# Performance work log

Measured on AMD Instinct MI355X. Metric: run time of the kernel, lower is better.

Reference implementation:

```python
import jax, jax.numpy as jnp
import numpy as np
import math

N, CIN, COUT, H, W, K = 8, 192, 192, 64, 64, 1024


def setup_inputs() -> dict:
    key = jax.random.key(0)
    k1, k2, k3, k4, k5 = jax.random.split(key, 5)
    latent = jax.random.normal(k1, (N, CIN, H, W), dtype=jnp.float32)
    # kaiming-uniform-like codebook init
    bound = math.sqrt(6.0 / COUT)
    codebook = jax.random.uniform(k2, (K, COUT), dtype=jnp.float32, minval=-bound, maxval=bound)
    # nn.Linear weights: [out_features, in_features]
    wq = jax.random.normal(k3, (COUT, CIN), dtype=jnp.float32) / math.sqrt(CIN)
    wk = jax.random.normal(k4, (COUT, COUT), dtype=jnp.float32) / math.sqrt(COUT)
    wv = jax.random.normal(k5, (COUT, COUT), dtype=jnp.float32) / math.sqrt(COUT)
    temperature1 = jnp.ones((), dtype=jnp.float32)
    return {"latent": latent, "codebook": codebook, "wq": wq, "wk": wk, "wv": wv,
            "temperature1": temperature1, "temperature": 1}


def reference(latent, codebook, wq, wk, wv, temperature1, temperature):
    # latent: [n, cin, h, w] -> q: [n, h, w, cout]
    q = jnp.einsum('nchw,oc->nhwo', latent, wq)
    k = codebook @ wk.T          # [K, cout]
    v = codebook @ wv.T          # [K, cout]
    scale = math.sqrt(CIN)
    # logit: [n, h, w, K]
    logit = jnp.einsum('nhwd,kd->nhwk', q, k) / scale * temperature1
    trueCode = jnp.argmax(logit, axis=-1)  # [n, h, w]
    # gumbel-softmax, hard=True (straight-through)
    gumbel = jax.random.gumbel(jax.random.key(42), logit.shape, dtype=logit.dtype)
    y_soft = jax.nn.softmax((logit + gumbel) / temperature, axis=-1)
    idx = jnp.argmax(y_soft, axis=-1)
    y_hard = jax.nn.one_hot(idx, K, dtype=logit.dtype)
    sample = y_hard + y_soft - jax.lax.stop_gradient(y_soft)
    # quantized: [n, h, w, cout] -> [n, cout, h, w]
    quantized = jnp.einsum('nhwk,kd->nhwd', sample, v).transpose(0, 3, 1, 2)
    return quantized, trueCode, logit
```

## Files before the change

kernel.cpp:

```cpp
#include <hip/hip_runtime.h>
#include <cstdint>
#include <cstddef>

#define CIN   192
#define COUT  192
#define KCB   1024
#define HWSZ  4096
#define NPIX  32768
#define LOGIT_SCALE_F 13.856406460551018f

#define QCOL0 832

__device__ __forceinline__ void threefry_0_42(uint32_t x0, uint32_t x1,
                                              uint32_t& o0, uint32_t& o1) {
  const uint32_t ks0 = 0u;
  const uint32_t ks1 = 42u;
  const uint32_t ks2 = 0x1BD11BDAu ^ 0u ^ 42u;
  x0 += ks0; x1 += ks1;
#define TFR(r) { x0 += x1; x1 = (x1 << (r)) | (x1 >> (32 - (r))); x1 ^= x0; }
  TFR(13) TFR(15) TFR(26) TFR(6)
  x0 += ks1; x1 += ks2 + 1u;
  TFR(17) TFR(29) TFR(16) TFR(24)
  x0 += ks2; x1 += ks0 + 2u;
  TFR(13) TFR(15) TFR(26) TFR(6)
  x0 += ks0; x1 += ks1 + 3u;
  TFR(17) TFR(29) TFR(16) TFR(24)
  x0 += ks1; x1 += ks2 + 4u;
  TFR(13) TFR(15) TFR(26) TFR(6)
  x0 += ks2; x1 += ks0 + 5u;
#undef TFR
  o0 = x0; o1 = x1;
}

__device__ __forceinline__ float gumbel_from_bits(uint32_t b) {
  float u = __uint_as_float((b >> 9) | 0x3F800000u) - 1.0f;
  u = fmaxf(u, 1.17549435e-38f);
  return -logf(-logf(u));
}

__global__ __launch_bounds__(192) void kv_kernel(
    const float* __restrict__ cb, const float* __restrict__ wk,
    const float* __restrict__ wv, float* __restrict__ km, float* __restrict__ vm) {
  __shared__ float4 row[48];
  const int j = blockIdx.x;
  const int o = threadIdx.x;
  if (o < 48) row[o] = reinterpret_cast<const float4*>(cb + (size_t)j * CIN)[o];
  __syncthreads();
  const float4* wkr = reinterpret_cast<const float4*>(wk + (size_t)o * CIN);
  const float4* wvr = reinterpret_cast<const float4*>(wv + (size_t)o * CIN);
  float sk = 0.f, sv = 0.f;
#pragma unroll 8
  for (int c = 0; c < 48; ++c) {
    float4 a = row[c];
    float4 b = wkr[c];
    float4 w = wvr[c];
    sk = fmaf(a.x, b.x, sk); sk = fmaf(a.y, b.y, sk);
    sk = fmaf(a.z, b.z, sk); sk = fmaf(a.w, b.w, sk);
    sv = fmaf(a.x, w.x, sv); sv = fmaf(a.y, w.y, sv);
    sv = fmaf(a.z, w.z, sv); sv = fmaf(a.w, w.w, sv);
  }
  km[(size_t)j * COUT + o] = sk;
  vm[(size_t)j * COUT + o] = sv;
}

__global__ __launch_bounds__(256) void q_kernel(
    const float* __restrict__ latent, const float* __restrict__ wq,
    float* __restrict__ logitq) {
  __shared__ float aT[16][68];
  __shared__ float bT[16][68];
  const int tid = threadIdx.x;
  const int p0 = blockIdx.x * 64;
  const int o0 = blockIdx.y * 64;
  const int n = p0 >> 12, hw0 = p0 & 4095;
  const float* lat = latent + (size_t)n * (CIN * HWSZ);
  const int tp = tid & 15, to = tid >> 4;
  float acc[4][4] = {};

  for (int c0 = 0; c0 < CIN; c0 += 16) {
    __syncthreads();
    {
      int px = tid & 63, cr = tid >> 6;
#pragma unroll
      for (int i = 0; i < 4; ++i) {
        int c = cr + i * 4;
        aT[c][px] = lat[(size_t)(c0 + c) * HWSZ + hw0 + px];
      }
      int tx = tid & 15, ty = tid >> 4;
#pragma unroll
      for (int i = 0; i < 4; ++i) {
        int o = ty * 4 + i;
        bT[tx][o] = wq[(size_t)(o0 + o) * CIN + c0 + tx];
      }
    }
    __syncthreads();
#pragma unroll
    for (int c = 0; c < 16; ++c) {
      float4 av = *reinterpret_cast<const float4*>(&aT[c][4 * tp]);
      float4 bv = *reinterpret_cast<const float4*>(&bT[c][4 * to]);
      acc[0][0] = fmaf(av.x, bv.x, acc[0][0]); acc[0][1] = fmaf(av.x, bv.y, acc[0][1]);
      acc[0][2] = fmaf(av.x, bv.z, acc[0][2]); acc[0][3] = fmaf(av.x, bv.w, acc[0][3]);
      acc[1][0] = fmaf(av.y, bv.x, acc[1][0]); acc[1][1] = fmaf(av.y, bv.y, acc[1][1]);
      acc[1][2] = fmaf(av.y, bv.z, acc[1][2]); acc[1][3] = fmaf(av.y, bv.w, acc[1][3]);
      acc[2][0] = fmaf(av.z, bv.x, acc[2][0]); acc[2][1] = fmaf(av.z, bv.y, acc[2][1]);
      acc[2][2] = fmaf(av.z, bv.z, acc[2][2]); acc[2][3] = fmaf(av.z, bv.w, acc[2][3]);
      acc[3][0] = fmaf(av.w, bv.x, acc[3][0]); acc[3][1] = fmaf(av.w, bv.y, acc[3][1]);
      acc[3][2] = fmaf(av.w, bv.z, acc[3][2]); acc[3][3] = fmaf(av.w, bv.w, acc[3][3]);
    }
  }
#pragma unroll
  for (int ii = 0; ii < 4; ++ii) {
    float4 w;
    w.x = acc[ii][0]; w.y = acc[ii][1]; w.z = acc[ii][2]; w.w = acc[ii][3];
    *reinterpret_cast<float4*>(logitq + (size_t)(p0 + 4 * tp + ii) * KCB + QCOL0 + o0 + 4 * to) = w;
  }
}

__global__ __launch_bounds__(256) void logit_kernel(
    const float* __restrict__ km, const float* __restrict__ vm,
    const float* __restrict__ t1p, float* __restrict__ logit_out,
    float* __restrict__ code_out, float* __restrict__ quant_out) {
  __shared__ float aT[CIN][68];
  __shared__ float bT[32][68];
  __shared__ float wLv[64][4];
  __shared__ int   wLi[64][4];
  __shared__ float wSv[64][4];
  __shared__ int   wSi[64][4];
  __shared__ int   sIdx[64];

  const int tid = threadIdx.x;
  const int p0 = blockIdx.x * 64;
  const float t1 = t1p[0];

  for (int i = 0; i < 12; ++i) {
    int flat = tid + i * 256;
    int r = flat / 48, c4 = flat % 48;
    float4 v = reinterpret_cast<const float4*>(
        logit_out + (size_t)(p0 + r) * KCB + QCOL0)[c4];
    aT[c4 * 4 + 0][r] = v.x;
    aT[c4 * 4 + 1][r] = v.y;
    aT[c4 * 4 + 2][r] = v.z;
    aT[c4 * 4 + 3][r] = v.w;
  }

  const int tp = tid & 15;
  const int to = tid >> 4;
  float Lv[4], Sv[4];
  int Li[4], Si[4];
#pragma unroll
  for (int ii = 0; ii < 4; ++ii) {
    Lv[ii] = -INFINITY; Sv[ii] = -INFINITY; Li[ii] = 0; Si[ii] = 0;
  }

  for (int jt = 0; jt < 16; ++jt) {
    float acc[4][4] = {};
    for (int c0 = 0; c0 < CIN; c0 += 32) {
      __syncthreads();
      {
        int c4 = tid & 7, jj = tid >> 3;
#pragma unroll
        for (int pass = 0; pass < 2; ++pass) {
          int jloc = jj + pass * 32;
          int jg = jt * 64 + jloc;
          float4 v = reinterpret_cast<const float4*>(km + (size_t)jg * CIN + c0)[c4];
          bT[c4 * 4 + 0][jloc] = v.x;
          bT[c4 * 4 + 1][jloc] = v.y;
          bT[c4 * 4 + 2][jloc] = v.z;
          bT[c4 * 4 + 3][jloc] = v.w;
        }
      }
      __syncthreads();
#pragma unroll
      for (int c = 0; c < 32; ++c) {
        float4 av = *reinterpret_cast<const float4*>(&aT[c0 + c][4 * tp]);
        float4 bv = *reinterpret_cast<const float4*>(&bT[c][4 * to]);
        acc[0][0] = fmaf(av.x, bv.x, acc[0][0]); acc[0][1] = fmaf(av.x, bv.y, acc[0][1]);
        acc[0][2] = fmaf(av.x, bv.z, acc[0][2]); acc[0][3] = fmaf(av.x, bv.w, acc[0][3]);
        acc[1][0] = fmaf(av.y, bv.x, acc[1][0]); acc[1][1] = fmaf(av.y, bv.y, acc[1][1]);
        acc[1][2] = fmaf(av.y, bv.z, acc[1][2]); acc[1][3] = fmaf(av.y, bv.w, acc[1][3]);
        acc[2][0] = fmaf(av.z, bv.x, acc[2][0]); acc[2][1] = fmaf(av.z, bv.y, acc[2][1]);
        acc[2][2] = fmaf(av.z, bv.z, acc[2][2]); acc[2][3] = fmaf(av.z, bv.w, acc[2][3]);
        acc[3][0] = fmaf(av.w, bv.x, acc[3][0]); acc[3][1] = fmaf(av.w, bv.y, acc[3][1]);
        acc[3][2] = fmaf(av.w, bv.z, acc[3][2]); acc[3][3] = fmaf(av.w, bv.w, acc[3][3]);
      }
    }
#pragma unroll
    for (int ii = 0; ii < 4; ++ii) {
      int p = p0 + 4 * tp + ii;
      int jb = jt * 64 + 4 * to;
      float4 lv;
      lv.x = acc[ii][0] / LOGIT_SCALE_F * t1;
      lv.y = acc[ii][1] / LOGIT_SCALE_F * t1;
      lv.z = acc[ii][2] / LOGIT_SCALE_F * t1;
      lv.w = acc[ii][3] / LOGIT_SCALE_F * t1;
      *reinterpret_cast<float4*>(logit_out + (size_t)p * KCB + jb) = lv;
      float vals[4] = {lv.x, lv.y, lv.z, lv.w};
#pragma unroll
      for (int jj = 0; jj < 4; ++jj) {
        int jgl = jb + jj;
        float val = vals[jj];
        if (val > Lv[ii]) { Lv[ii] = val; Li[ii] = jgl; }
        uint32_t b0, b1;
        threefry_0_42(0u, (uint32_t)p * (uint32_t)KCB + (uint32_t)jgl, b0, b1);
        float s = val + gumbel_from_bits(b0 ^ b1);
        if (s > Sv[ii]) { Sv[ii] = s; Si[ii] = jgl; }
      }
    }
  }

  {
    const int lane = tid & 63;
    const int wvid = tid >> 6;
#pragma unroll
    for (int ii = 0; ii < 4; ++ii) {
      float v = Lv[ii]; int idx = Li[ii];
      float s = Sv[ii]; int sidx = Si[ii];
#pragma unroll
      for (int m = 16; m <= 32; m <<= 1) {
        float v2 = __shfl_xor(v, m); int i2 = __shfl_xor(idx, m);
        if (v2 > v || (v2 == v && i2 < idx)) { v = v2; idx = i2; }
        float s2 = __shfl_xor(s, m); int j2 = __shfl_xor(sidx, m);
        if (s2 > s || (s2 == s && j2 < sidx)) { s = s2; sidx = j2; }
      }
      if (lane < 16) {
        int r = 4 * tp + ii;
        wLv[r][wvid] = v; wLi[r][wvid] = idx;
        wSv[r][wvid] = s; wSi[r][wvid] = sidx;
      }
    }
  }
  __syncthreads();
  if (tid < 64) {
    int r = tid;
    float bv = wLv[r][0]; int bi = wLi[r][0];
    float sv = wSv[r][0]; int si = wSi[r][0];
#pragma unroll
    for (int t = 1; t < 4; ++t) {
      float v1 = wLv[r][t]; int i1 = wLi[r][t];
      if (v1 > bv || (v1 == bv && i1 < bi)) { bv = v1; bi = i1; }
      float v2 = wSv[r][t]; int i2 = wSi[r][t];
      if (v2 > sv || (v2 == sv && i2 < si)) { sv = v2; si = i2; }
    }
    code_out[p0 + r] = (float)bi;
    sIdx[r] = si;
  }
  __syncthreads();

  {
    int l = tid & 63, dg = tid >> 6;
    int p = p0 + l;
    int n = p >> 12, hw = p & 4095;
    int jv = sIdx[l];
    const float* vrow = vm + (size_t)jv * COUT;
    float* qb = quant_out + (size_t)n * (COUT * HWSZ) + hw;
#pragma unroll
    for (int it = 0; it < 48; ++it) {
      int d = it * 4 + dg;
      qb[(size_t)d * HWSZ] = vrow[d];
    }
  }
}

extern "C" void kernel_launch(void* const* d_in, const int* in_sizes, int n_in,
                              void* d_out, int out_size, void* d_ws, size_t ws_size,
                              hipStream_t stream) {
  (void)in_sizes; (void)n_in; (void)out_size; (void)ws_size;
  const float* latent   = (const float*)d_in[0];
  const float* codebook = (const float*)d_in[1];
  const float* wq       = (const float*)d_in[2];
  const float* wk       = (const float*)d_in[3];
  const float* wv       = (const float*)d_in[4];
  const float* t1       = (const float*)d_in[5];

  float* ws = (float*)d_ws;
  float* km = ws;
  float* vm = ws + 196608;

  float* quant = (float*)d_out;
  float* code  = quant + 6291456;
  float* logit = code + 32768;

  kv_kernel<<<dim3(KCB), dim3(192), 0, stream>>>(codebook, wk, wv, km, vm);
  q_kernel<<<dim3(NPIX / 64, CIN / 64), dim3(256), 0, stream>>>(latent, wq, logit);
  logit_kernel<<<dim3(NPIX / 64), dim3(256), 0, stream>>>(km, vm, t1, logit, code, quant);
}
```

Baseline: 563.8 us.

## Fuse Q projection into logit kernel and double-buffer codebook key tiles

Computes the per-pixel Q projection directly into shared memory inside the logit kernel, removing the separate q_kernel and the scratch round-trip through the logit output buffer. It also double-buffers the key tile loads with register prefetch so global loads overlap the FMA loop, cutting one barrier per step, and adds a launch-bounds occupancy hint. In exchange each block recomputes Q for its 64 pixels, and the larger shared footprint plus prefetch registers may limit occupancy.

After: 872.3 us. 54.7% more time.

```diff
diff --git a/kernel.cpp b/kernel.cpp
--- a/kernel.cpp
+++ b/kernel.cpp
@@ -8,8 +8,6 @@
 #define HWSZ  4096
 #define NPIX  32768
 #define LOGIT_SCALE_F 13.856406460551018f
-
-#define QCOL0 832
 
 __device__ __forceinline__ void threefry_0_42(uint32_t x0, uint32_t x1,
                                               uint32_t& o0, uint32_t& o1) {
@@ -37,6 +35,17 @@
   u = fmaxf(u, 1.17549435e-38f);
   return -logf(-logf(u));
 }
+
+#define FMA16(acc, av, bv) do { \
+  acc[0][0]=fmaf(av.x,bv.x,acc[0][0]); acc[0][1]=fmaf(av.x,bv.y,acc[0][1]); \
+  acc[0][2]=fmaf(av.x,bv.z,acc[0][2]); acc[0][3]=fmaf(av.x,bv.w,acc[0][3]); \
+  acc[1][0]=fmaf(av.y,bv.x,acc[1][0]); acc[1][1]=fmaf(av.y,bv.y,acc[1][1]); \
+  acc[1][2]=fmaf(av.y,bv.z,acc[1][2]); acc[1][3]=fmaf(av.y,bv.w,acc[1][3]); \
+  acc[2][0]=fmaf(av.z,bv.x,acc[2][0]); acc[2][1]=fmaf(av.z,bv.y,acc[2][1]); \
+  acc[2][2]=fmaf(av.z,bv.z,acc[2][2]); acc[2][3]=fmaf(av.z,bv.w,acc[2][3]); \
+  acc[3][0]=fmaf(av.w,bv.x,acc[3][0]); acc[3][1]=fmaf(av.w,bv.y,acc[3][1]); \
+  acc[3][2]=fmaf(av.w,bv.z,acc[3][2]); acc[3][3]=fmaf(av.w,bv.w,acc[3][3]); \
+} while (0)
 
 __global__ __launch_bounds__(192) void kv_kernel(
     const float* __restrict__ cb, const float* __restrict__ wk,
@@ -63,64 +72,13 @@
   vm[(size_t)j * COUT + o] = sv;
 }
 
-__global__ __launch_bounds__(256) void q_kernel(
+__global__ __launch_bounds__(256, 2) void fused_kernel(
     const float* __restrict__ latent, const float* __restrict__ wq,
-    float* __restrict__ logitq) {
-  __shared__ float aT[16][68];
-  __shared__ float bT[16][68];
-  const int tid = threadIdx.x;
-  const int p0 = blockIdx.x * 64;
-  const int o0 = blockIdx.y * 64;
-  const int n = p0 >> 12, hw0 = p0 & 4095;
-  const float* lat = latent + (size_t)n * (CIN * HWSZ);
-  const int tp = tid & 15, to = tid >> 4;
-  float acc[4][4] = {};
-
-  for (int c0 = 0; c0 < CIN; c0 += 16) {
-    __syncthreads();
-    {
-      int px = tid & 63, cr = tid >> 6;
-#pragma unroll
-      for (int i = 0; i < 4; ++i) {
-        int c = cr + i * 4;
-        aT[c][px] = lat[(size_t)(c0 + c) * HWSZ + hw0 + px];
-      }
-      int tx = tid & 15, ty = tid >> 4;
-#pragma unroll
-      for (int i = 0; i < 4; ++i) {
-        int o = ty * 4 + i;
-        bT[tx][o] = wq[(size_t)(o0 + o) * CIN + c0 + tx];
-      }
-    }
-    __syncthreads();
-#pragma unroll
-    for (int c = 0; c < 16; ++c) {
-      float4 av = *reinterpret_cast<const float4*>(&aT[c][4 * tp]);
-      float4 bv = *reinterpret_cast<const float4*>(&bT[c][4 * to]);
-      acc[0][0] = fmaf(av.x, bv.x, acc[0][0]); acc[0][1] = fmaf(av.x, bv.y, acc[0][1]);
-      acc[0][2] = fmaf(av.x, bv.z, acc[0][2]); acc[0][3] = fmaf(av.x, bv.w, acc[0][3]);
-      acc[1][0] = fmaf(av.y, bv.x, acc[1][0]); acc[1][1] = fmaf(av.y, bv.y, acc[1][1]);
-      acc[1][2] = fmaf(av.y, bv.z, acc[1][2]); acc[1][3] = fmaf(av.y, bv.w, acc[1][3]);
-      acc[2][0] = fmaf(av.z, bv.x, acc[2][0]); acc[2][1] = fmaf(av.z, bv.y, acc[2][1]);
-      acc[2][2] = fmaf(av.z, bv.z, acc[2][2]); acc[2][3] = fmaf(av.z, bv.w, acc[2][3]);
-      acc[3][0] = fmaf(av.w, bv.x, acc[3][0]); acc[3][1] = fmaf(av.w, bv.y, acc[3][1]);
-      acc[3][2] = fmaf(av.w, bv.z, acc[3][2]); acc[3][3] = fmaf(av.w, bv.w, acc[3][3]);
-    }
-  }
-#pragma unroll
-  for (int ii = 0; ii < 4; ++ii) {
-    float4 w;
-    w.x = acc[ii][0]; w.y = acc[ii][1]; w.z = acc[ii][2]; w.w = acc[ii][3];
-    *reinterpret_cast<float4*>(logitq + (size_t)(p0 + 4 * tp + ii) * KCB + QCOL0 + o0 + 4 * to) = w;
-  }
-}
-
-__global__ __launch_bounds__(256) void logit_kernel(
     const float* __restrict__ km, const float* __restrict__ vm,
     const float* __restrict__ t1p, float* __restrict__ logit_out,
     float* __restrict__ code_out, float* __restrict__ quant_out) {
   __shared__ float aT[CIN][68];
-  __shared__ float bT[32][68];
+  __shared__ float bT[2][32][68];
   __shared__ float wLv[64][4];
   __shared__ int   wLi[64][4];
   __shared__ float wSv[64][4];
@@ -129,21 +87,49 @@
 
   const int tid = threadIdx.x;
   const int p0 = blockIdx.x * 64;
+  const int n = p0 >> 12, hw0 = p0 & 4095;
   const float t1 = t1p[0];
-
-  for (int i = 0; i < 12; ++i) {
-    int flat = tid + i * 256;
-    int r = flat / 48, c4 = flat % 48;
-    float4 v = reinterpret_cast<const float4*>(
-        logit_out + (size_t)(p0 + r) * KCB + QCOL0)[c4];
-    aT[c4 * 4 + 0][r] = v.x;
-    aT[c4 * 4 + 1][r] = v.y;
-    aT[c4 * 4 + 2][r] = v.z;
-    aT[c4 * 4 + 3][r] = v.w;
-  }
-
   const int tp = tid & 15;
   const int to = tid >> 4;
+
+  {
+    const float4* lat4 =
+        reinterpret_cast<const float4*>(latent + (size_t)n * (CIN * HWSZ));
+    const float4* wq4 = reinterpret_cast<const float4*>(wq);
+    const int hw40 = hw0 >> 2;
+    const int lf = tid & 15, lr = tid >> 4;
+    const int wc4 = tid & 7, wr = tid >> 3;
+    for (int ot = 0; ot < 3; ++ot) {
+      const int o0 = ot * 64;
+      float acc[4][4] = {};
+      for (int c0 = 0; c0 < CIN; c0 += 32) {
+        float4 l0 = lat4[(size_t)(c0 + lr) * (HWSZ / 4) + hw40 + lf];
+        float4 l1 = lat4[(size_t)(c0 + lr + 16) * (HWSZ / 4) + hw40 + lf];
+        float4 w0 = wq4[(size_t)(o0 + wr) * (CIN / 4) + (c0 >> 2) + wc4];
+        float4 w1 = wq4[(size_t)(o0 + wr + 32) * (CIN / 4) + (c0 >> 2) + wc4];
+        __syncthreads();
+        *reinterpret_cast<float4*>(&bT[0][lr][4 * lf]) = l0;
+        *reinterpret_cast<float4*>(&bT[0][lr + 16][4 * lf]) = l1;
+        bT[1][4 * wc4 + 0][wr] = w0.x; bT[1][4 * wc4 + 1][wr] = w0.y;
+        bT[1][4 * wc4 + 2][wr] = w0.z; bT[1][4 * wc4 + 3][wr] = w0.w;
+        bT[1][4 * wc4 + 0][wr + 32] = w1.x; bT[1][4 * wc4 + 1][wr + 32] = w1.y;
+        bT[1][4 * wc4 + 2][wr + 32] = w1.z; bT[1][4 * wc4 + 3][wr + 32] = w1.w;
+        __syncthreads();
+#pragma unroll
+        for (int c = 0; c < 32; ++c) {
+          float4 av = *reinterpret_cast<const float4*>(&bT[0][c][4 * tp]);
+          float4 bv = *reinterpret_cast<const float4*>(&bT[1][c][4 * to]);
+          FMA16(acc, av, bv);
+        }
+      }
+#pragma unroll
+      for (int ii = 0; ii < 4; ++ii)
+#pragma unroll
+        for (int kk = 0; kk < 4; ++kk)
+          aT[o0 + 4 * to + kk][4 * tp + ii] = acc[ii][kk];
+    }
+  }
+
   float Lv[4], Sv[4];
   int Li[4], Si[4];
 #pragma unroll
@@ -151,42 +137,51 @@
     Lv[ii] = -INFINITY; Sv[ii] = -INFINITY; Li[ii] = 0; Si[ii] = 0;
   }
 
+  const float4* km4 = reinterpret_cast<const float4*>(km);
+  const int sc4 = tid & 7, sjj = tid >> 3;
+
+  {
+    float4 n0 = km4[(size_t)sjj * 48 + sc4];
+    float4 n1 = km4[(size_t)(sjj + 32) * 48 + sc4];
+    __syncthreads();
+    bT[0][4 * sc4 + 0][sjj] = n0.x; bT[0][4 * sc4 + 1][sjj] = n0.y;
+    bT[0][4 * sc4 + 2][sjj] = n0.z; bT[0][4 * sc4 + 3][sjj] = n0.w;
+    bT[0][4 * sc4 + 0][sjj + 32] = n1.x; bT[0][4 * sc4 + 1][sjj + 32] = n1.y;
+    bT[0][4 * sc4 + 2][sjj + 32] = n1.z; bT[0][4 * sc4 + 3][sjj + 32] = n1.w;
+  }
+
   for (int jt = 0; jt < 16; ++jt) {
     float acc[4][4] = {};
-    for (int c0 = 0; c0 < CIN; c0 += 32) {
+    for (int ci = 0; ci < 6; ++ci) {
+      const int k = jt * 6 + ci;
+      float4 n0, n1;
+      const bool pref = (k + 1 < 96);
+      if (pref) {
+        const int njt = (k + 1) / 6, nc0 = ((k + 1) % 6) * 32;
+        n0 = km4[(size_t)(njt * 64 + sjj) * 48 + (nc0 >> 2) + sc4];
+        n1 = km4[(size_t)(njt * 64 + sjj + 32) * 48 + (nc0 >> 2) + sc4];
+      }
       __syncthreads();
-      {
-        int c4 = tid & 7, jj = tid >> 3;
-#pragma unroll
-        for (int pass = 0; pass < 2; ++pass) {
-          int jloc = jj + pass * 32;
-          int jg = jt * 64 + jloc;
-          float4 v = reinterpret_cast<const float4*>(km + (size_t)jg * CIN + c0)[c4];
-          bT[c4 * 4 + 0][jloc] = v.x;
-          bT[c4 * 4 + 1][jloc] = v.y;
-          bT[c4 * 4 + 2][jloc] = v.z;
-          bT[c4 * 4 + 3][jloc] = v.w;
-        }
-      }
-      __syncthreads();
+      const int c0 = ci * 32;
+      const int cur = k & 1;
 #pragma unroll
       for (int c = 0; c < 32; ++c) {
         float4 av = *reinterpret_cast<const float4*>(&aT[c0 + c][4 * tp]);
-        float4 bv = *reinterpret_cast<const float4*>(&bT[c][4 * to]);
-        acc[0][0] = fmaf(av.x, bv.x, acc[0][0]); acc[0][1] = fmaf(av.x, bv.y, acc[0][1]);
-        acc[0][2] = fmaf(av.x, bv.z, acc[0][2]); acc[0][3] = fmaf(av.x, bv.w, acc[0][3]);
-        acc[1][0] = fmaf(av.y, bv.x, acc[1][0]); acc[1][1] = fmaf(av.y, bv.y, acc[1][1]);
-        acc[1][2] = fmaf(av.y, bv.z, acc[1][2]); acc[1][3] = fmaf(av.y, bv.w, acc[1][3]);
-        acc[2][0] = fmaf(av.z, bv.x, acc[2][0]); acc[2][1] = fmaf(av.z, bv.y, acc[2][1]);
-        acc[2][2] = fmaf(av.z, bv.z, acc[2][2]); acc[2][3] = fmaf(av.z, bv.w, acc[2][3]);
-        acc[3][0] = fmaf(av.w, bv.x, acc[3][0]); acc[3][1] = fmaf(av.w, bv.y, acc[3][1]);
-        acc[3][2] = fmaf(av.w, bv.z, acc[3][2]); acc[3][3] = fmaf(av.w, bv.w, acc[3][3]);
+        float4 bv = *reinterpret_cast<const float4*>(&bT[cur][c][4 * to]);
+        FMA16(acc, av, bv);
+      }
+      if (pref) {
+        const int b = cur ^ 1;
+        bT[b][4 * sc4 + 0][sjj] = n0.x; bT[b][4 * sc4 + 1][sjj] = n0.y;
+        bT[b][4 * sc4 + 2][sjj] = n0.z; bT[b][4 * sc4 + 3][sjj] = n0.w;
+        bT[b][4 * sc4 + 0][sjj + 32] = n1.x; bT[b][4 * sc4 + 1][sjj + 32] = n1.y;
+        bT[b][4 * sc4 + 2][sjj + 32] = n1.z; bT[b][4 * sc4 + 3][sjj + 32] = n1.w;
       }
     }
 #pragma unroll
     for (int ii = 0; ii < 4; ++ii) {
-      int p = p0 + 4 * tp + ii;
-      int jb = jt * 64 + 4 * to;
+      const int p = p0 + 4 * tp + ii;
+      const int jb = jt * 64 + 4 * to;
       float4 lv;
       lv.x = acc[ii][0] / LOGIT_SCALE_F * t1;
       lv.y = acc[ii][1] / LOGIT_SCALE_F * t1;
@@ -196,12 +191,12 @@
       float vals[4] = {lv.x, lv.y, lv.z, lv.w};
 #pragma unroll
       for (int jj = 0; jj < 4; ++jj) {
-        int jgl = jb + jj;
-        float val = vals[jj];
+        const int jgl = jb + jj;
+        const float val = vals[jj];
         if (val > Lv[ii]) { Lv[ii] = val; Li[ii] = jgl; }
         uint32_t b0, b1;
         threefry_0_42(0u, (uint32_t)p * (uint32_t)KCB + (uint32_t)jgl, b0, b1);
-        float s = val + gumbel_from_bits(b0 ^ b1);
+        const float s = val + gumbel_from_bits(b0 ^ b1);
         if (s > Sv[ii]) { Sv[ii] = s; Si[ii] = jgl; }
       }
     }
@@ -222,7 +217,7 @@
         if (s2 > s || (s2 == s && j2 < sidx)) { s = s2; sidx = j2; }
       }
       if (lane < 16) {
-        int r = 4 * tp + ii;
+        const int r = 4 * tp + ii;
         wLv[r][wvid] = v; wLi[r][wvid] = idx;
         wSv[r][wvid] = s; wSi[r][wvid] = sidx;
       }
@@ -230,7 +225,7 @@
   }
   __syncthreads();
   if (tid < 64) {
-    int r = tid;
+    const int r = tid;
     float bv = wLv[r][0]; int bi = wLi[r][0];
     float sv = wSv[r][0]; int si = wSi[r][0];
 #pragma unroll
@@ -246,15 +241,15 @@
   __syncthreads();
 
   {
-    int l = tid & 63, dg = tid >> 6;
-    int p = p0 + l;
-    int n = p >> 12, hw = p & 4095;
-    int jv = sIdx[l];
+    const int l = tid & 63, dg = tid >> 6;
+    const int p = p0 + l;
+    const int nn = p >> 12, hw = p & 4095;
+    const int jv = sIdx[l];
     const float* vrow = vm + (size_t)jv * COUT;
-    float* qb = quant_out + (size_t)n * (COUT * HWSZ) + hw;
+    float* qb = quant_out + (size_t)nn * (COUT * HWSZ) + hw;
 #pragma unroll
     for (int it = 0; it < 48; ++it) {
-      int d = it * 4 + dg;
+      const int d = it * 4 + dg;
       qb[(size_t)d * HWSZ] = vrow[d];
     }
   }
@@ -280,6 +275,6 @@
   float* logit = code + 32768;
 
   kv_kernel<<<dim3(KCB), dim3(192), 0, stream>>>(codebook, wk, wv, km, vm);
-  q_kernel<<<dim3(NPIX / 64, CIN / 64), dim3(256), 0, stream>>>(latent, wq, logit);
-  logit_kernel<<<dim3(NPIX / 64), dim3(256), 0, stream>>>(km, vm, t1, logit, code, quant);
-}
+  fused_kernel<<<dim3(NPIX / 64), dim3(256), 0, stream>>>(
+      latent, wq, km, vm, t1, logit, code, quant);
+}
```
